# Performance work log

Hardware: AMD Instinct MI355X
Metric: run time of the kernel (lower is better)

Reference implementation:

```python
import jax, jax.numpy as jnp
import numpy as np

N, E = 25000, 400000
F, D, H, C, L = 64, 128, 4, 128, 3  # in_feat, hidden, heads, per-head dim, layers
SCALE = 1.0 / np.sqrt(C)

_PNAMES = [f"{nm}{l}" for l in range(L) for nm in ("Wq", "bq", "Wk", "bk", "Wv", "bv", "Ws", "bs")]


def setup_inputs() -> dict:
    key = jax.random.key(0)
    ks = jax.random.split(key, 64)
    inp = {
        "x": jax.random.normal(ks[0], (N, F), jnp.float32),
        "edge_index": jax.random.randint(ks[1], (2, E), 0, N, jnp.int32),
    }
    i = 2
    for l in range(L):
        fin = F if l == 0 else D
        s = 1.0 / np.sqrt(fin)
        shapes = {"Wq": (fin, H * C), "bq": (H * C,), "Wk": (fin, H * C), "bk": (H * C,),
                  "Wv": (fin, H * C), "bv": (H * C,), "Ws": (fin, D), "bs": (D,)}
        for nm, shp in shapes.items():
            scale = s if nm.startswith("W") else 0.01
            inp[f"{nm}{l}"] = jax.random.normal(ks[i], shp, jnp.float32) * scale
            i += 1
    inp["Wfc"] = jax.random.normal(ks[i], (D, 1), jnp.float32) * (1.0 / np.sqrt(D))
    inp["bfc"] = jnp.zeros((1,), jnp.float32)
    return inp


def _conv(x, src, dst, Wq, bq, Wk, bk, Wv, bv, Ws, bs):
    """PyG TransformerConv, heads=H, concat=False (head-mean), root_weight=True."""
    n = x.shape[0]
    q = (x @ Wq + bq).reshape(n, H, C)
    k = (x @ Wk + bk).reshape(n, H, C)
    v = (x @ Wv + bv).reshape(n, H, C)
    # per-edge attention logits: query at dst, key at src  -> [E, H]
    alpha = jnp.einsum("ehc,ehc->eh", q[dst], k[src]) * SCALE
    # scatter-softmax over incoming edges of each destination node
    m = jax.ops.segment_max(alpha, dst, num_segments=n)        # [N, H]
    e = jnp.exp(alpha - m[dst])                                 # [E, H]
    denom = jax.ops.segment_sum(e, dst, num_segments=n)        # [N, H]
    a = e / (denom[dst] + 1e-16)                                # [E, H]
    out = jax.ops.segment_sum(a[:, :, None] * v[src], dst, num_segments=n)  # [N, H, C]
    return out.mean(axis=1) + x @ Ws + bs                       # concat=False -> mean heads; + skip


def reference(x, edge_index,
              Wq0, bq0, Wk0, bk0, Wv0, bv0, Ws0, bs0,
              Wq1, bq1, Wk1, bk1, Wv1, bv1, Ws1, bs1,
              Wq2, bq2, Wk2, bk2, Wv2, bv2, Ws2, bs2,
              Wfc, bfc):
    src, dst = edge_index[0], edge_index[1]
    h = jax.nn.relu(_conv(x, src, dst, Wq0, bq0, Wk0, bk0, Wv0, bv0, Ws0, bs0))
    h = jax.nn.relu(_conv(h, src, dst, Wq1, bq1, Wk1, bk1, Wv1, bv1, Ws1, bs1))
    h = jax.nn.relu(_conv(h, src, dst, Wq2, bq2, Wk2, bk2, Wv2, bv2, Ws2, bs2))
    g = h.mean(axis=0, keepdims=True)                           # [1, D]
    return jax.nn.sigmoid(g @ Wfc + bfc)                        # [1, 1]
```

## Files before the change

### kernel.cpp

```cpp
#include <hip/hip_runtime.h>
#include <hip/hip_bf16.h>
#include <math.h>

#define NNODES 25000
#define NEDGES 400000
#define FIN0 64
#define DHID 128
#define NHEAD 4
#define CDIM 128
#define HC (NHEAD * CDIM)
#define NOUT 1664
#define SCALE 0.088388347648318447f

typedef __attribute__((ext_vector_type(8))) short short8;
typedef __attribute__((ext_vector_type(4))) float floatx4;
typedef __attribute__((ext_vector_type(2))) float fx2;

__device__ __forceinline__ short f2bf(float v) {
    unsigned u = __float_as_uint(v);
    u = (u + 0x7fffu + ((u >> 16) & 1u)) >> 16;
    return (short)u;
}
__device__ __forceinline__ float bf2f(short s) {
    return __uint_as_float(((unsigned)(unsigned short)s) << 16);
}


__global__ void zero_int_kernel(int* __restrict__ p, int n) {
    int i = blockIdx.x * blockDim.x + threadIdx.x;
    if (i < n) p[i] = 0;
}

__global__ void zero_float_kernel(float* __restrict__ p, int n) {
    int i = blockIdx.x * blockDim.x + threadIdx.x;
    if (i < n) p[i] = 0.f;
}

__global__ void cvt_x_kernel(const float* __restrict__ x, short* __restrict__ xb, int total) {
    int i = blockIdx.x * blockDim.x + threadIdx.x;
    if (i < total) xb[i] = f2bf(x[i]);
}

__global__ void cvt_w_kernel(const float* __restrict__ Wq, const float* __restrict__ Wk,
                             const float* __restrict__ Wv, const float* __restrict__ Ws,
                             const float* __restrict__ bq, const float* __restrict__ bk,
                             const float* __restrict__ bv, const float* __restrict__ bs,
                             short* __restrict__ WT, float* __restrict__ bc, int finShift) {
    int idx = blockIdx.x * blockDim.x + threadIdx.x;
    int fin = 1 << finShift;
    int total = NOUT << finShift;
    if (idx < total) {
        int c = idx >> finShift;
        int k = idx & (fin - 1);
        float v;
        if (c < 512)       v = Wq[k * 512 + c];
        else if (c < 1024) v = Wk[k * 512 + c - 512];
        else if (c < 1536) v = Wv[k * 512 + c - 1024];
        else               v = Ws[k * 128 + c - 1536];
        WT[idx] = f2bf(v);
    }
    if (idx < NOUT) {
        int c = idx;
        float b;
        if (c < 512)       b = bq[c];
        else if (c < 1024) b = bk[c - 512];
        else if (c < 1536) b = bv[c - 1024];
        else               b = bs[c - 1536];
        bc[c] = b;
    }
}


__global__ void count_kernel(const int* __restrict__ dst, int* __restrict__ deg, int e) {
    int i = blockIdx.x * blockDim.x + threadIdx.x;
    if (i < e) atomicAdd(&deg[dst[i]], 1);
}

__global__ void scan_kernel(const int* __restrict__ deg, int* __restrict__ offs,
                            int* __restrict__ cnt, int n, int total) {
    __shared__ int sums[256];
    int t = threadIdx.x;
    int chunk = (n + 255) / 256;
    int b = t * chunk;
    int e = min(b + chunk, n);
    int s = 0;
    for (int i = b; i < e; ++i) s += deg[i];
    sums[t] = s;
    __syncthreads();
    for (int o = 1; o < 256; o <<= 1) {
        int v = (t >= o) ? sums[t - o] : 0;
        __syncthreads();
        sums[t] += v;
        __syncthreads();
    }
    int run = sums[t] - s;
    for (int i = b; i < e; ++i) {
        offs[i] = run;
        run += deg[i];
        cnt[i] = 0;
    }
    if (t == 0) offs[n] = total;
}

__global__ void scatter_kernel(const int* __restrict__ src, const int* __restrict__ dst,
                               const int* __restrict__ offs, int* __restrict__ cnt,
                               int* __restrict__ csr, int e) {
    int i = blockIdx.x * blockDim.x + threadIdx.x;
    if (i < e) {
        int d = dst[i];
        int pos = offs[d] + atomicAdd(&cnt[d], 1);
        csr[pos] = src[i];
    }
}

template<int FIN>
__global__ __launch_bounds__(256) void gemm_qkvs_mfma(
    const short* __restrict__ Xb, int n,
    const short* __restrict__ WT, const float* __restrict__ bc,
    short* __restrict__ Qb, unsigned char* __restrict__ KV,
    short* __restrict__ Sb)
{
    constexpr int PITCH = FIN + 8;
    constexpr int CSH = (FIN == 128) ? 4 : 3;
    constexpr int CMASK = (1 << CSH) - 1;

    __shared__ short Xs[128][PITCH];
    __shared__ short Wt[128][PITCH];

    int t = threadIdx.x;
    int row0 = blockIdx.x * 128;
    int y = blockIdx.y;
    int col0 = y * 128;

    for (int i = t; i < (128 << CSH); i += 256) {
        int r = i >> CSH, c = (i & CMASK) * 8;
        int gr = row0 + r;
        uint4 v = make_uint4(0u, 0u, 0u, 0u);
        if (gr < n) v = *(const uint4*)&Xb[(size_t)gr * FIN + c];
        *(uint4*)&Xs[r][c] = v;
    }
    for (int i = t; i < (128 << CSH); i += 256) {
        int r = i >> CSH, c = (i & CMASK) * 8;
        *(uint4*)&Wt[r][c] = *(const uint4*)&WT[(size_t)(col0 + r) * FIN + c];
    }
    __syncthreads();

    int l = t & 63, w = t >> 6;
    int wr = (w >> 1) * 64, wc = (w & 1) * 64;
    int lr = l & 15, lk = (l >> 4) * 8;

    floatx4 acc[4][4] = {};
    for (int k0 = 0; k0 < FIN; k0 += 32) {
        short8 a[4], b[4];
#pragma unroll
        for (int mi = 0; mi < 4; ++mi)
            a[mi] = *(const short8*)&Xs[wr + mi * 16 + lr][k0 + lk];
#pragma unroll
        for (int ni = 0; ni < 4; ++ni)
            b[ni] = *(const short8*)&Wt[wc + ni * 16 + lr][k0 + lk];
#pragma unroll
        for (int mi = 0; mi < 4; ++mi)
#pragma unroll
            for (int ni = 0; ni < 4; ++ni)
                acc[mi][ni] = __builtin_amdgcn_mfma_f32_16x16x32_bf16(
                    a[mi], b[ni], acc[mi][ni], 0, 0, 0);
    }

    int rb = (l >> 4) * 4, cl = l & 15;
    int kind = (y < 4) ? 0 : (y < 8) ? 1 : (y < 12) ? 2 : 3;
#pragma unroll
    for (int mi = 0; mi < 4; ++mi) {
#pragma unroll
        for (int ni = 0; ni < 4; ++ni) {
            int gc = col0 + wc + ni * 16 + cl;
            float bias = bc[gc];
#pragma unroll
            for (int r = 0; r < 4; ++r) {
                int gr = row0 + wr + mi * 16 + rb + r;
                if (gr >= n) continue;
                float v = acc[mi][ni][r] + bias;
                if (kind == 0) {
                    Qb[(size_t)gr * 512 + gc] = f2bf(v);
                } else if (kind == 1) {
                    unsigned enc = (unsigned)__builtin_amdgcn_cvt_pk_fp8_f32(v, v, 0, false);
                    KV[(size_t)gr * 1024 + (gc - 512)] = (unsigned char)enc;
                } else if (kind == 2) {
                    unsigned enc = (unsigned)__builtin_amdgcn_cvt_pk_fp8_f32(v, v, 0, false);
                    KV[(size_t)gr * 1024 + 512 + (gc - 1024)] = (unsigned char)enc;
                } else {
                    Sb[(size_t)gr * 128 + (gc - 1536)] = f2bf(v);
                }
            }
        }
    }
}


__device__ __forceinline__ void unpack8(uint4 r, float* f) {
    f[0] = __uint_as_float(r.x << 16);
    f[1] = __uint_as_float(r.x & 0xffff0000u);
    f[2] = __uint_as_float(r.y << 16);
    f[3] = __uint_as_float(r.y & 0xffff0000u);
    f[4] = __uint_as_float(r.z << 16);
    f[5] = __uint_as_float(r.z & 0xffff0000u);
    f[6] = __uint_as_float(r.w << 16);
    f[7] = __uint_as_float(r.w & 0xffff0000u);
}

__device__ __forceinline__ void decf8(uint2 r, float* f) {
    fx2 a = __builtin_amdgcn_cvt_pk_f32_fp8(r.x, false);
    fx2 b = __builtin_amdgcn_cvt_pk_f32_fp8(r.x, true);
    fx2 c = __builtin_amdgcn_cvt_pk_f32_fp8(r.y, false);
    fx2 d = __builtin_amdgcn_cvt_pk_f32_fp8(r.y, true);
    f[0] = a[0]; f[1] = a[1]; f[2] = b[0]; f[3] = b[1];
    f[4] = c[0]; f[5] = c[1]; f[6] = d[0]; f[7] = d[1];
}

__device__ __forceinline__ float dotf8(const float* q, uint2 r) {
    float f[8];
    decf8(r, f);
    float p = 0.f;
#pragma unroll
    for (int j = 0; j < 8; ++j) p = fmaf(q[j], f[j], p);
    return p;
}

__device__ __forceinline__ void updf8(float& m, float& d, float* acc,
                                      float alpha, uint2 vr) {
    float vf[8];
    decf8(vr, vf);
    float nm = fmaxf(m, alpha);
    float sc = __expf(m - nm);
    float w  = __expf(alpha - nm);
    d = d * sc + w;
#pragma unroll
    for (int j = 0; j < 8; ++j) acc[j] = acc[j] * sc + w * vf[j];
    m = nm;
}

__global__ __launch_bounds__(256) void attn_kernel(
    const short* __restrict__ Qb, const unsigned char* __restrict__ KV,
    const int* __restrict__ offs, const int* __restrict__ csr,
    const short* __restrict__ Sb, short* __restrict__ Xo, int n)
{
    int node = (blockIdx.x * blockDim.x + threadIdx.x) >> 6;
    if (node >= n) return;
    int lane = threadIdx.x & 63;

    float qf[8];
    {
        uint4 qr = *(const uint4*)&Qb[(size_t)node * 512 + lane * 8];
        unpack8(qr, qf);
    }

    int beg = offs[node], end = offs[node + 1];
    float m = -INFINITY, d = 0.f;
    float acc[8] = {};

    int e = beg;
    for (; e + 3 < end; e += 4) {
        int s0 = csr[e], s1 = csr[e + 1], s2 = csr[e + 2], s3 = csr[e + 3];
        const unsigned char* b0 = KV + (size_t)s0 * 1024 + lane * 8;
        const unsigned char* b1 = KV + (size_t)s1 * 1024 + lane * 8;
        const unsigned char* b2 = KV + (size_t)s2 * 1024 + lane * 8;
        const unsigned char* b3 = KV + (size_t)s3 * 1024 + lane * 8;
        uint2 k0 = *(const uint2*)b0;
        uint2 k1 = *(const uint2*)b1;
        uint2 k2 = *(const uint2*)b2;
        uint2 k3 = *(const uint2*)b3;
        uint2 v0 = *(const uint2*)(b0 + 512);
        uint2 v1 = *(const uint2*)(b1 + 512);
        uint2 v2 = *(const uint2*)(b2 + 512);
        uint2 v3 = *(const uint2*)(b3 + 512);
        float p0 = dotf8(qf, k0);
        float p1 = dotf8(qf, k1);
        float p2 = dotf8(qf, k2);
        float p3 = dotf8(qf, k3);
#pragma unroll
        for (int o = 1; o < 16; o <<= 1) {
            p0 += __shfl_xor(p0, o);
            p1 += __shfl_xor(p1, o);
            p2 += __shfl_xor(p2, o);
            p3 += __shfl_xor(p3, o);
        }
        updf8(m, d, acc, p0 * SCALE, v0);
        updf8(m, d, acc, p1 * SCALE, v1);
        updf8(m, d, acc, p2 * SCALE, v2);
        updf8(m, d, acc, p3 * SCALE, v3);
    }
    for (; e < end; ++e) {
        int s0 = csr[e];
        const unsigned char* b0 = KV + (size_t)s0 * 1024 + lane * 8;
        uint2 k0 = *(const uint2*)b0;
        uint2 v0 = *(const uint2*)(b0 + 512);
        float p0 = dotf8(qf, k0);
#pragma unroll
        for (int o = 1; o < 16; o <<= 1) p0 += __shfl_xor(p0, o);
        updf8(m, d, acc, p0 * SCALE, v0);
    }

    float inv = (d > 0.f) ? 1.f / d : 0.f;
#pragma unroll
    for (int j = 0; j < 8; ++j) acc[j] *= inv;

#pragma unroll
    for (int j = 0; j < 8; ++j) {
        acc[j] += __shfl_xor(acc[j], 16);
        acc[j] += __shfl_xor(acc[j], 32);
    }

    if (lane < 16) {
        int c0 = lane * 8;
        float sf[8];
        uint4 sr = *(const uint4*)&Sb[(size_t)node * 128 + c0];
        unpack8(sr, sf);
        short8 o;
#pragma unroll
        for (int j = 0; j < 8; ++j)
            o[j] = f2bf(fmaxf(acc[j] * 0.25f + sf[j], 0.f));
        *(short8*)&Xo[(size_t)node * 128 + c0] = o;
    }
}

__global__ void colsum_kernel(const short* __restrict__ X, float* __restrict__ g, int n) {
    int c = threadIdx.x;
    int rpb = (n + gridDim.x - 1) / gridDim.x;
    int r0 = blockIdx.x * rpb;
    int r1 = min(r0 + rpb, n);
    float acc = 0.f;
    for (int r = r0; r < r1; ++r) acc += bf2f(X[r * DHID + c]);
    atomicAdd(&g[c], acc);
}

__global__ void final_kernel(const float* __restrict__ g, const float* __restrict__ Wfc,
                             const float* __restrict__ bfc, float* __restrict__ out, float invn) {
    __shared__ float red[128];
    int t = threadIdx.x;
    red[t] = g[t] * invn * Wfc[t];
    __syncthreads();
    for (int o = 64; o > 0; o >>= 1) {
        if (t < o) red[t] += red[t + o];
        __syncthreads();
    }
    if (t == 0) {
        float z = red[0] + bfc[0];
        out[0] = 1.f / (1.f + expf(-z));
    }
}


extern "C" void kernel_launch(void* const* d_in, const int* in_sizes, int n_in,
                              void* d_out, int out_size, void* d_ws, size_t ws_size,
                              hipStream_t stream) {
    const int N = NNODES, E = NEDGES;
    const float* x = (const float*)d_in[0];
    const int* ei = (const int*)d_in[1];
    const int* src = ei;
    const int* dst = ei + E;
    const float* Wfc = (const float*)d_in[26];
    const float* bfc = (const float*)d_in[27];

    size_t off = 0;
    auto alloc = [&](size_t bytes) -> char* {
        char* p = (char*)d_ws + off;
        off += (bytes + 255) & ~(size_t)255;
        return p;
    };
    int* deg   = (int*)alloc((size_t)N * 4);
    int* cnt   = (int*)alloc((size_t)N * 4);
    int* offs  = (int*)alloc((size_t)(N + 1) * 4);
    int* csr   = (int*)alloc((size_t)E * 4);
    short* Qb  = (short*)alloc((size_t)N * HC * 2);
    unsigned char* KV = (unsigned char*)alloc((size_t)N * 1024);
    short* Sb  = (short*)alloc((size_t)N * DHID * 2);
    short* xb0 = (short*)alloc((size_t)N * FIN0 * 2);
    short* xb1 = (short*)alloc((size_t)N * DHID * 2);
    short* xb2 = (short*)alloc((size_t)N * DHID * 2);
    short* WT  = (short*)alloc((size_t)NOUT * DHID * 2);
    float* bc  = (float*)alloc((size_t)NOUT * 4);
    float* g   = (float*)alloc(128 * 4);

    zero_int_kernel<<<(N + 255) / 256, 256, 0, stream>>>(deg, N);
    zero_float_kernel<<<1, 128, 0, stream>>>(g, 128);
    count_kernel<<<(E + 255) / 256, 256, 0, stream>>>(dst, deg, E);
    scan_kernel<<<1, 256, 0, stream>>>(deg, offs, cnt, N, E);
    scatter_kernel<<<(E + 255) / 256, 256, 0, stream>>>(src, dst, offs, cnt, csr, E);

    cvt_x_kernel<<<(N * FIN0 + 255) / 256, 256, 0, stream>>>(x, xb0, N * FIN0);

    int attn_blocks = (N + 3) / 4;

    const short* xin = xb0;
    short* xouts[3] = { xb1, xb2, xb1 };
    for (int l = 0; l < 3; ++l) {
        int finShift = (l == 0) ? 6 : 7;
        int fin = 1 << finShift;
        const float* Wq = (const float*)d_in[2 + l * 8 + 0];
        const float* bq = (const float*)d_in[2 + l * 8 + 1];
        const float* Wk = (const float*)d_in[2 + l * 8 + 2];
        const float* bk = (const float*)d_in[2 + l * 8 + 3];
        const float* Wv = (const float*)d_in[2 + l * 8 + 4];
        const float* bv = (const float*)d_in[2 + l * 8 + 5];
        const float* Wss= (const float*)d_in[2 + l * 8 + 6];
        const float* bs = (const float*)d_in[2 + l * 8 + 7];

        cvt_w_kernel<<<(NOUT * fin + 255) / 256, 256, 0, stream>>>(
            Wq, Wk, Wv, Wss, bq, bk, bv, bs, WT, bc, finShift);

        dim3 ggrid((N + 127) / 128, 13);
        if (l == 0)
            gemm_qkvs_mfma<64><<<ggrid, 256, 0, stream>>>(xin, N, WT, bc, Qb, KV, Sb);
        else
            gemm_qkvs_mfma<128><<<ggrid, 256, 0, stream>>>(xin, N, WT, bc, Qb, KV, Sb);
        attn_kernel<<<attn_blocks, 256, 0, stream>>>(Qb, KV, offs, csr, Sb, xouts[l], N);
        xin = xouts[l];
    }

    colsum_kernel<<<256, 128, 0, stream>>>(xb1, g, N);
    final_kernel<<<1, 128, 0, stream>>>(g, Wfc, bfc, (float*)d_out, 1.0f / N);
}
```

Baseline: 609.5 us.

## Retile QKVS GEMM to 64-row tiles with weights read directly from global

```diff
diff --git a/kernel.cpp b/kernel.cpp
--- a/kernel.cpp
+++ b/kernel.cpp
@@ -26,14 +26,10 @@
 }
 
 
-__global__ void zero_int_kernel(int* __restrict__ p, int n) {
+__global__ void zero_ws_kernel(int* __restrict__ deg, float* __restrict__ g, int n) {
     int i = blockIdx.x * blockDim.x + threadIdx.x;
-    if (i < n) p[i] = 0;
-}
-
-__global__ void zero_float_kernel(float* __restrict__ p, int n) {
-    int i = blockIdx.x * blockDim.x + threadIdx.x;
-    if (i < n) p[i] = 0.f;
+    if (i < n) deg[i] = 0;
+    if (i < 128) g[i] = 0.f;
 }
 
 __global__ void cvt_x_kernel(const float* __restrict__ x, short* __restrict__ xb, int total) {
@@ -121,43 +117,42 @@
     short* __restrict__ Sb)
 {
     constexpr int PITCH = FIN + 8;
-    constexpr int CSH = (FIN == 128) ? 4 : 3;
-    constexpr int CMASK = (1 << CSH) - 1;
-
-    __shared__ short Xs[128][PITCH];
-    __shared__ short Wt[128][PITCH];
+    constexpr int CPR = FIN / 8;
+    __shared__ short Xs[64][PITCH];
 
     int t = threadIdx.x;
-    int row0 = blockIdx.x * 128;
-    int y = blockIdx.y;
-    int col0 = y * 128;
-
-    for (int i = t; i < (128 << CSH); i += 256) {
-        int r = i >> CSH, c = (i & CMASK) * 8;
+    int row0 = blockIdx.x * 64;
+    int col0 = blockIdx.y * 256;
+
+    for (int i = t; i < 64 * CPR; i += 256) {
+        int r = i / CPR, c = (i % CPR) * 8;
         int gr = row0 + r;
         uint4 v = make_uint4(0u, 0u, 0u, 0u);
         if (gr < n) v = *(const uint4*)&Xb[(size_t)gr * FIN + c];
         *(uint4*)&Xs[r][c] = v;
     }
-    for (int i = t; i < (128 << CSH); i += 256) {
-        int r = i >> CSH, c = (i & CMASK) * 8;
-        *(uint4*)&Wt[r][c] = *(const uint4*)&WT[(size_t)(col0 + r) * FIN + c];
-    }
     __syncthreads();
 
     int l = t & 63, w = t >> 6;
-    int wr = (w >> 1) * 64, wc = (w & 1) * 64;
+    int wcol = col0 + w * 64;
+    if (wcol >= NOUT) return;
     int lr = l & 15, lk = (l >> 4) * 8;
+    int cl = l & 15, rb = (l >> 4) * 4;
+
+    float bias[4];
+#pragma unroll
+    for (int ni = 0; ni < 4; ++ni) bias[ni] = bc[wcol + ni * 16 + cl];
 
     floatx4 acc[4][4] = {};
     for (int k0 = 0; k0 < FIN; k0 += 32) {
-        short8 a[4], b[4];
+        short8 b[4];
+#pragma unroll
+        for (int ni = 0; ni < 4; ++ni)
+            b[ni] = *(const short8*)&WT[(size_t)(wcol + ni * 16 + lr) * FIN + k0 + lk];
+        short8 a[4];
 #pragma unroll
         for (int mi = 0; mi < 4; ++mi)
-            a[mi] = *(const short8*)&Xs[wr + mi * 16 + lr][k0 + lk];
-#pragma unroll
-        for (int ni = 0; ni < 4; ++ni)
-            b[ni] = *(const short8*)&Wt[wc + ni * 16 + lr][k0 + lk];
+            a[mi] = *(const short8*)&Xs[mi * 16 + lr][k0 + lk];
 #pragma unroll
         for (int mi = 0; mi < 4; ++mi)
 #pragma unroll
@@ -166,19 +161,17 @@
                     a[mi], b[ni], acc[mi][ni], 0, 0, 0);
     }
 
-    int rb = (l >> 4) * 4, cl = l & 15;
-    int kind = (y < 4) ? 0 : (y < 8) ? 1 : (y < 12) ? 2 : 3;
+    int kind = (wcol < 512) ? 0 : (wcol < 1024) ? 1 : (wcol < 1536) ? 2 : 3;
 #pragma unroll
     for (int mi = 0; mi < 4; ++mi) {
 #pragma unroll
         for (int ni = 0; ni < 4; ++ni) {
-            int gc = col0 + wc + ni * 16 + cl;
-            float bias = bc[gc];
+            int gc = wcol + ni * 16 + cl;
 #pragma unroll
             for (int r = 0; r < 4; ++r) {
-                int gr = row0 + wr + mi * 16 + rb + r;
+                int gr = row0 + mi * 16 + rb + r;
                 if (gr >= n) continue;
-                float v = acc[mi][ni][r] + bias;
+                float v = acc[mi][ni][r] + bias[ni];
                 if (kind == 0) {
                     Qb[(size_t)gr * 512 + gc] = f2bf(v);
                 } else if (kind == 1) {
@@ -380,8 +373,7 @@
     float* bc  = (float*)alloc((size_t)NOUT * 4);
     float* g   = (float*)alloc(128 * 4);
 
-    zero_int_kernel<<<(N + 255) / 256, 256, 0, stream>>>(deg, N);
-    zero_float_kernel<<<1, 128, 0, stream>>>(g, 128);
+    zero_ws_kernel<<<(N + 255) / 256, 256, 0, stream>>>(deg, g, N);
     count_kernel<<<(E + 255) / 256, 256, 0, stream>>>(dst, deg, E);
     scan_kernel<<<1, 256, 0, stream>>>(deg, offs, cnt, N, E);
     scatter_kernel<<<(E + 255) / 256, 256, 0, stream>>>(src, dst, offs, cnt, csr, E);
@@ -407,7 +399,7 @@
         cvt_w_kernel<<<(NOUT * fin + 255) / 256, 256, 0, stream>>>(
             Wq, Wk, Wv, Wss, bq, bk, bv, bs, WT, bc, finShift);
 
-        dim3 ggrid((N + 127) / 128, 13);
+        dim3 ggrid((N + 63) / 64, 7);
         if (l == 0)
             gemm_qkvs_mfma<64><<<ggrid, 256, 0, stream>>>(xin, N, WT, bc, Qb, KV, Sb);
         else
```

Result: faster. 590.1 us (-3.2%).
